# Kernel optimization log

Hardware: AMD Instinct MI355X
Metric: run time of the kernel (lower is better)

## Reference

```python
import jax, jax.numpy as jnp
import numpy as np

NEG_SLOPE = 0.2


def setup_inputs() -> dict:
    key = jax.random.key(0)
    ks = jax.random.split(key, 10)
    V, E, Din, Dout, H = 50000, 800000, 128, 128, 4
    h = jax.random.normal(ks[0], (V, Din), dtype=jnp.float32)
    edge_index = jax.random.randint(ks[1], (2, E), 0, V, dtype=jnp.int32)
    edge_weight = jax.random.uniform(ks[2], (E,), dtype=jnp.float32)
    s = 1.0 / np.sqrt(Din)
    Wq = jax.random.normal(ks[3], (Din, Dout), dtype=jnp.float32) * s
    Wk = jax.random.normal(ks[4], (Din, Dout), dtype=jnp.float32) * s
    Wv = jax.random.normal(ks[5], (Din, Dout), dtype=jnp.float32) * s
    Wo = jax.random.normal(ks[6], (Dout, Dout), dtype=jnp.float32) * (1.0 / np.sqrt(Dout))
    We = jax.random.normal(ks[7], (1, H), dtype=jnp.float32)
    bq = jnp.zeros((Dout,), jnp.float32)
    bk = jnp.zeros((Dout,), jnp.float32)
    bv = jnp.zeros((Dout,), jnp.float32)
    bo = jnp.zeros((Dout,), jnp.float32)
    be = jnp.zeros((H,), jnp.float32)
    return {"h": h, "edge_index": edge_index, "edge_weight": edge_weight,
            "Wq": Wq, "bq": bq, "Wk": Wk, "bk": bk, "Wv": Wv, "bv": bv,
            "Wo": Wo, "bo": bo, "We": We, "be": be}


def reference(h, edge_index, edge_weight, Wq, bq, Wk, bk, Wv, bv, Wo, bo, We, be):
    V = h.shape[0]
    H = be.shape[0]
    Dout = Wq.shape[1]
    F_h = Dout // H

    # Node projections -> [V, H, F_h]
    Q = (h @ Wq + bq).reshape(V, H, F_h)
    K = (h @ Wk + bk).reshape(V, H, F_h)
    Vv = (h @ Wv + bv).reshape(V, H, F_h)

    # Edge bias: Linear(1, H) on edge_weight, then LeakyReLU -> [E, H]
    edge_bias = jax.nn.leaky_relu(edge_weight[:, None] @ We + be, negative_slope=NEG_SLOPE)

    src, tgt = edge_index[0], edge_index[1]

    # Per-edge attention logits: dot(Q[src], K[tgt]) / sqrt(F_h) + bias -> [E, H]
    attn_raw = jnp.sum(Q[src] * K[tgt], axis=-1) / jnp.sqrt(jnp.float32(F_h)) + edge_bias
    attn_exp = jnp.exp(attn_raw)  # faithful: original uses unshifted exp

    # Scatter-softmax normalizer per target node -> [V, H]
    deg = jax.ops.segment_sum(attn_exp, tgt, num_segments=V) + 1e-16
    attn_norm = attn_exp / deg[tgt]  # [E, H]

    # Weighted messages and scatter-sum to targets
    msg = Vv[src] * attn_norm[:, :, None] * edge_weight[:, None, None]  # [E, H, F_h]
    out = jax.ops.segment_sum(msg, tgt, num_segments=V)  # [V, H, F_h]

    out = out.reshape(V, H * F_h)
    out = jax.nn.leaky_relu(out @ Wo + bo, negative_slope=NEG_SLOPE)
    return out
```

## Files before the change

### kernel.cpp

```cpp
#include <hip/hip_runtime.h>
#include <hip/hip_bf16.h>

#define NEG_SLOPE 0.2f

__global__ __launch_bounds__(256) void gemm_big(
    const float* __restrict__ A,
    const float* __restrict__ W0, const float* __restrict__ W1, const float* __restrict__ W2,
    const float* __restrict__ b0, const float* __restrict__ b1, const float* __restrict__ b2,
    float* __restrict__ D0, float* __restrict__ D1, float* __restrict__ D2,
    int V, int lrelu)
{
    __shared__ float As[16][136];
    __shared__ float Bs[16][192];

    const int m = blockIdx.y;
    const float* __restrict__ W  = (m == 0) ? W0 : ((m == 1) ? W1 : W2);
    const float* __restrict__ bb = (m == 0) ? b0 : ((m == 1) ? b1 : b2);
    float* __restrict__ D        = (m == 0) ? D0 : ((m == 1) ? D1 : D2);

    const int tid = threadIdx.x;
    const int tx = tid & 15;
    const int ty = tid >> 4;
    const int row0 = blockIdx.x * 128;

    const int ar = tid >> 1;
    const int ak = (tid & 1) * 8;
    const int bk = tid >> 4;
    const int bc = tid & 15;

    float acc[8][8];
#pragma unroll
    for (int i = 0; i < 8; ++i)
#pragma unroll
        for (int j = 0; j < 8; ++j) acc[i][j] = 0.f;

    for (int k0 = 0; k0 < 128; k0 += 16) {
        {
            const int gr = row0 + ar;
            float4 a0 = make_float4(0.f, 0.f, 0.f, 0.f);
            float4 a1 = make_float4(0.f, 0.f, 0.f, 0.f);
            if (gr < V) {
                a0 = *(const float4*)(A + (size_t)gr * 128 + k0 + ak);
                a1 = *(const float4*)(A + (size_t)gr * 128 + k0 + ak + 4);
            }
            As[ak + 0][ar] = a0.x; As[ak + 1][ar] = a0.y;
            As[ak + 2][ar] = a0.z; As[ak + 3][ar] = a0.w;
            As[ak + 4][ar] = a1.x; As[ak + 5][ar] = a1.y;
            As[ak + 6][ar] = a1.z; As[ak + 7][ar] = a1.w;
        }
        {
            const float4 w0 = *(const float4*)(W + (size_t)(k0 + bk) * 128 + bc * 8);
            const float4 w1 = *(const float4*)(W + (size_t)(k0 + bk) * 128 + bc * 8 + 4);
            *(float4*)&Bs[bk][bc * 12]     = w0;
            *(float4*)&Bs[bk][bc * 12 + 4] = w1;
        }
        __syncthreads();
#pragma unroll
        for (int kk = 0; kk < 16; ++kk) {
            float a[8], b[8];
            *(float4*)&a[0] = *(const float4*)&As[kk][ty * 8];
            *(float4*)&a[4] = *(const float4*)&As[kk][ty * 8 + 4];
            *(float4*)&b[0] = *(const float4*)&Bs[kk][tx * 12];
            *(float4*)&b[4] = *(const float4*)&Bs[kk][tx * 12 + 4];
#pragma unroll
            for (int i = 0; i < 8; ++i)
#pragma unroll
                for (int j = 0; j < 8; ++j) acc[i][j] = fmaf(a[i], b[j], acc[i][j]);
        }
        __syncthreads();
    }

#pragma unroll
    for (int i = 0; i < 8; ++i) {
        const int gr = row0 + ty * 8 + i;
        if (gr >= V) continue;
#pragma unroll
        for (int j = 0; j < 8; j += 4) {
            float4 o;
            float* op = &o.x;
#pragma unroll
            for (int jj = 0; jj < 4; ++jj) {
                float x = acc[i][j + jj] + bb[tx * 8 + j + jj];
                if (lrelu) x = (x > 0.f) ? x : NEG_SLOPE * x;
                op[jj] = x;
            }
            *(float4*)(D + (size_t)gr * 128 + tx * 8 + j) = o;
        }
    }
}

__global__ __launch_bounds__(256) void count_tgt(const int* __restrict__ tgt,
                                                 int* __restrict__ cnt, int E)
{
    const int e = blockIdx.x * blockDim.x + threadIdx.x;
    if (e < E) atomicAdd(cnt + tgt[e], 1);
}

__global__ __launch_bounds__(256) void scan1(const int* __restrict__ cnt,
                                             int* __restrict__ offs,
                                             int* __restrict__ bsums, int V)
{
    __shared__ int sh[256];
    const int t = threadIdx.x;
    const int base = blockIdx.x * 1024;
    int v[4];
    int s = 0;
#pragma unroll
    for (int i = 0; i < 4; ++i) {
        const int idx = base + t * 4 + i;
        v[i] = (idx < V) ? cnt[idx] : 0;
        s += v[i];
    }
    sh[t] = s;
    __syncthreads();
    for (int off = 1; off < 256; off <<= 1) {
        const int x = (t >= off) ? sh[t - off] : 0;
        __syncthreads();
        sh[t] += x;
        __syncthreads();
    }
    int run = (t > 0) ? sh[t - 1] : 0;
#pragma unroll
    for (int i = 0; i < 4; ++i) {
        const int idx = base + t * 4 + i;
        if (idx < V) offs[idx] = run;
        run += v[i];
    }
    if (t == 255) bsums[blockIdx.x] = sh[255];
}

__global__ void scan2(int* __restrict__ bsums, int nb)
{
    if (threadIdx.x == 0 && blockIdx.x == 0) {
        int run = 0;
        for (int i = 0; i < nb; ++i) { const int x = bsums[i]; bsums[i] = run; run += x; }
    }
}

__global__ __launch_bounds__(256) void scan3(int* __restrict__ offs,
                                             const int* __restrict__ bsums,
                                             int* __restrict__ fill, int V)
{
    const int v = blockIdx.x * blockDim.x + threadIdx.x;
    if (v >= V) return;
    const int o = offs[v] + bsums[v >> 10];
    offs[v] = o;
    fill[v] = o;
}

__global__ __launch_bounds__(256) void scatter_edges(
    const int* __restrict__ src, const int* __restrict__ tgt,
    const float* __restrict__ ew, int* __restrict__ fill,
    int2* __restrict__ se, int E)
{
    const int e = blockIdx.x * blockDim.x + threadIdx.x;
    if (e >= E) return;
    const int pos = atomicAdd(fill + tgt[e], 1);
    se[pos] = make_int2(src[e], __float_as_int(ew[e]));
}

__global__ __launch_bounds__(256) void fused_agg(
    const float* __restrict__ Q, const float* __restrict__ K,
    const float* __restrict__ Vv, const int2* __restrict__ se,
    const int* __restrict__ offs, const int* __restrict__ fill,
    const float* __restrict__ Wei, const float* __restrict__ bei,
    float* __restrict__ accum, int V)
{
    __shared__ float Ksh[4][4][36];
    const int wid = threadIdx.x >> 6;
    const int node = blockIdx.x * 4 + wid;
    if (node >= V) return;
    const int l   = threadIdx.x & 63;
    const int h   = l & 3;
    const int hd  = l >> 4;
    const float weH = Wei[h], beH = bei[h];
    const float2* __restrict__ Vv2 = (const float2*)Vv;

    {
        const float2 kk = *(const float2*)(K + (size_t)node * 128 + l * 2);
        const int f0 = l * 2;
        Ksh[wid][f0 >> 5][f0 & 31] = kk.x;
        Ksh[wid][(f0 + 1) >> 5][(f0 + 1) & 31] = kk.y;
    }

    const int start = offs[node];
    const int end   = fill[node];

    float degacc = 0.f;
    float ax = 0.f, ay = 0.f;

    for (int b0 = start; b0 < end; b0 += 16) {
        const int nj = min(16, end - b0);
        const int jj = l >> 2;
        int   s = 0;
        float w = 0.f, p = 0.f;
        if (jj < nj) {
            const int2 t = se[b0 + jj];
            s = t.x;
            w = __int_as_float(t.y);
            const float4* qp = (const float4*)(Q + (size_t)s * 128 + h * 32);
            float dot = 0.f;
#pragma unroll
            for (int i = 0; i < 8; ++i) {
                const float4 q = qp[i];
                const float4 k = *(const float4*)&Ksh[wid][h][i * 4];
                dot += q.x * k.x + q.y * k.y + q.z * k.z + q.w * k.w;
            }
            float bb = fmaf(w, weH, beH);
            bb = (bb > 0.f) ? bb : NEG_SLOPE * bb;
            p = __expf(fmaf(dot, 0.17677669529663687f, bb));
        }
        degacc += p;
        const float coef = p * w;

        if (nj == 16) {
#pragma unroll
            for (int j = 0; j < 16; ++j) {
                const float cj = __shfl(coef, j * 4 + hd);
                const int   sj = __shfl(s,    j * 4);
                const float2 v = Vv2[(size_t)sj * 64 + l];
                ax = fmaf(cj, v.x, ax);
                ay = fmaf(cj, v.y, ay);
            }
        } else {
            for (int j = 0; j < nj; ++j) {
                const float cj = __shfl(coef, j * 4 + hd);
                const int   sj = __shfl(s,    j * 4);
                const float2 v = Vv2[(size_t)sj * 64 + l];
                ax = fmaf(cj, v.x, ax);
                ay = fmaf(cj, v.y, ay);
            }
        }
    }

    float d = degacc;
    d += __shfl_xor(d, 4);
    d += __shfl_xor(d, 8);
    d += __shfl_xor(d, 16);
    d += __shfl_xor(d, 32);
    const float deg = __shfl(d, hd);
    const float inv = 1.0f / (deg + 1e-16f);

    *(float2*)(accum + (size_t)node * 128 + l * 2) =
        make_float2(ax * inv, ay * inv);
}

extern "C" void kernel_launch(void* const* d_in, const int* in_sizes, int n_in,
                              void* d_out, int out_size, void* d_ws, size_t ws_size,
                              hipStream_t stream)
{
    const float* h   = (const float*)d_in[0];
    const int*   ei  = (const int*)  d_in[1];
    const float* ew  = (const float*)d_in[2];
    const float* Wq  = (const float*)d_in[3];
    const float* bq  = (const float*)d_in[4];
    const float* Wk  = (const float*)d_in[5];
    const float* bk  = (const float*)d_in[6];
    const float* Wv  = (const float*)d_in[7];
    const float* bv  = (const float*)d_in[8];
    const float* Wo  = (const float*)d_in[9];
    const float* bo  = (const float*)d_in[10];
    const float* Wei = (const float*)d_in[11];
    const float* bei = (const float*)d_in[12];

    const int V = in_sizes[0] / 128;
    const int E = in_sizes[2];
    const int* src = ei;
    const int* tgt = ei + E;

    float* Q     = (float*)d_ws;
    float* Km    = Q  + (size_t)V * 128;
    float* Vm    = Km + (size_t)V * 128;
    float* accum = Vm + (size_t)V * 128;
    int2*  se    = (int2*)(accum + (size_t)V * 128);
    int*   cnt   = (int*)(se + E);
    int*   offs  = cnt  + V;
    int*   fill  = offs + V + 1;
    int*   bsums = fill + V;

    hipMemsetAsync(cnt, 0, (size_t)V * sizeof(int), stream);

    const int bigGrid = (V + 127) / 128;
    gemm_big<<<dim3(bigGrid, 3), 256, 0, stream>>>(
        h, Wq, Wk, Wv, bq, bk, bv, Q, Km, Vm, V, 0);

    count_tgt<<<(E + 255) / 256, 256, 0, stream>>>(tgt, cnt, E);
    const int nb = (V + 1023) / 1024;
    scan1<<<nb, 256, 0, stream>>>(cnt, offs, bsums, V);
    scan2<<<1, 64, 0, stream>>>(bsums, nb);
    scan3<<<(V + 255) / 256, 256, 0, stream>>>(offs, bsums, fill, V);
    scatter_edges<<<(E + 255) / 256, 256, 0, stream>>>(
        src, tgt, ew, fill, se, E);

    fused_agg<<<(V + 3) / 4, 256, 0, stream>>>(
        Q, Km, Vm, se, offs, fill, Wei, bei, accum, V);

    gemm_big<<<dim3(bigGrid, 1), 256, 0, stream>>>(
        accum, Wo, Wo, Wo, bo, bo, bo, (float*)d_out, (float*)d_out, (float*)d_out, V, 1);
}
```

Baseline: 319.0 us.

## Split aggregation per head so each wavefront handles one node-head pair

```diff
diff --git a/kernel.cpp b/kernel.cpp
--- a/kernel.cpp
+++ b/kernel.cpp
@@ -159,90 +159,85 @@
     se[pos] = make_int2(src[e], __float_as_int(ew[e]));
 }
 
-__global__ __launch_bounds__(256) void fused_agg(
+__global__ __launch_bounds__(256) void fused_agg_h(
     const float* __restrict__ Q, const float* __restrict__ K,
     const float* __restrict__ Vv, const int2* __restrict__ se,
     const int* __restrict__ offs, const int* __restrict__ fill,
     const float* __restrict__ Wei, const float* __restrict__ bei,
     float* __restrict__ accum, int V)
 {
-    __shared__ float Ksh[4][4][36];
-    const int wid = threadIdx.x >> 6;
-    const int node = blockIdx.x * 4 + wid;
+    const int head  = blockIdx.x & 3;
+    const int chunk = blockIdx.x >> 2;
+    const int wid   = threadIdx.x >> 6;
+    const int node  = chunk * 4 + wid;
     if (node >= V) return;
     const int l   = threadIdx.x & 63;
-    const int h   = l & 3;
-    const int hd  = l >> 4;
-    const float weH = Wei[h], beH = bei[h];
-    const float2* __restrict__ Vv2 = (const float2*)Vv;
-
-    {
-        const float2 kk = *(const float2*)(K + (size_t)node * 128 + l * 2);
-        const int f0 = l * 2;
-        Ksh[wid][f0 >> 5][f0 & 31] = kk.x;
-        Ksh[wid][(f0 + 1) >> 5][(f0 + 1) & 31] = kk.y;
-    }
-
-    const int start = offs[node];
-    const int end   = fill[node];
+    const int eg  = l >> 2;
+    const int qi  = l & 3;
+    const int grp = l >> 4;
+    const int d   = l & 15;
+
+    const float4* kp = (const float4*)(K + (size_t)node * 128 + head * 32);
+    const float4 k0 = kp[qi * 2];
+    const float4 k1 = kp[qi * 2 + 1];
+
+    const float weH = Wei[head], beH = bei[head];
+
+    int b0 = offs[node];
+    const int e0 = fill[node];
 
     float degacc = 0.f;
     float ax = 0.f, ay = 0.f;
 
-    for (int b0 = start; b0 < end; b0 += 16) {
-        const int nj = min(16, end - b0);
-        const int jj = l >> 2;
-        int   s = 0;
-        float w = 0.f, p = 0.f;
-        if (jj < nj) {
-            const int2 t = se[b0 + jj];
-            s = t.x;
-            w = __int_as_float(t.y);
-            const float4* qp = (const float4*)(Q + (size_t)s * 128 + h * 32);
-            float dot = 0.f;
-#pragma unroll
-            for (int i = 0; i < 8; ++i) {
-                const float4 q = qp[i];
-                const float4 k = *(const float4*)&Ksh[wid][h][i * 4];
-                dot += q.x * k.x + q.y * k.y + q.z * k.z + q.w * k.w;
+    for (; b0 < e0; b0 += 16) {
+        const int nj = min(16, e0 - b0);
+        int s_raw = 0; float w_raw = 0.f;
+        if (l < nj) {
+            const int2 t = se[b0 + l];
+            s_raw = t.x; w_raw = __int_as_float(t.y);
+        }
+        const int   s = __shfl(s_raw, eg);
+        const float w = __shfl(w_raw, eg);
+
+        float p = 0.f;
+        {
+            const float4* qp = (const float4*)(Q + (size_t)s * 128 + head * 32);
+            const float4 q0 = qp[qi * 2];
+            const float4 q1 = qp[qi * 2 + 1];
+            float dot = q0.x * k0.x + q0.y * k0.y + q0.z * k0.z + q0.w * k0.w
+                      + q1.x * k1.x + q1.y * k1.y + q1.z * k1.z + q1.w * k1.w;
+            dot += __shfl_xor(dot, 1);
+            dot += __shfl_xor(dot, 2);
+            if (eg < nj) {
+                float bb = fmaf(w, weH, beH);
+                bb = (bb > 0.f) ? bb : NEG_SLOPE * bb;
+                p = __expf(fmaf(dot, 0.17677669529663687f, bb));
             }
-            float bb = fmaf(w, weH, beH);
-            bb = (bb > 0.f) ? bb : NEG_SLOPE * bb;
-            p = __expf(fmaf(dot, 0.17677669529663687f, bb));
         }
         degacc += p;
         const float coef = p * w;
 
-        if (nj == 16) {
-#pragma unroll
-            for (int j = 0; j < 16; ++j) {
-                const float cj = __shfl(coef, j * 4 + hd);
-                const int   sj = __shfl(s,    j * 4);
-                const float2 v = Vv2[(size_t)sj * 64 + l];
-                ax = fmaf(cj, v.x, ax);
-                ay = fmaf(cj, v.y, ay);
-            }
-        } else {
-            for (int j = 0; j < nj; ++j) {
-                const float cj = __shfl(coef, j * 4 + hd);
-                const int   sj = __shfl(s,    j * 4);
-                const float2 v = Vv2[(size_t)sj * 64 + l];
-                ax = fmaf(cj, v.x, ax);
-                ay = fmaf(cj, v.y, ay);
-            }
-        }
-    }
-
-    float d = degacc;
-    d += __shfl_xor(d, 4);
-    d += __shfl_xor(d, 8);
-    d += __shfl_xor(d, 16);
-    d += __shfl_xor(d, 32);
-    const float deg = __shfl(d, hd);
-    const float inv = 1.0f / (deg + 1e-16f);
-
-    *(float2*)(accum + (size_t)node * 128 + l * 2) =
-        make_float2(ax * inv, ay * inv);
+        for (int j = 0; j < nj; j += 4) {
+            const int   e  = j + grp;
+            const float cj = __shfl(coef, e * 4);
+            const int   sj = __shfl(s,    e * 4);
+            const float2 v = *(const float2*)(Vv + (size_t)sj * 128 + head * 32 + d * 2);
+            ax = fmaf(cj, v.x, ax);
+            ay = fmaf(cj, v.y, ay);
+        }
+    }
+
+    ax += __shfl_xor(ax, 16); ax += __shfl_xor(ax, 32);
+    ay += __shfl_xor(ay, 16); ay += __shfl_xor(ay, 32);
+    float dg = degacc;
+    dg += __shfl_xor(dg, 1);  dg += __shfl_xor(dg, 2);
+    dg += __shfl_xor(dg, 4);  dg += __shfl_xor(dg, 8);
+    dg += __shfl_xor(dg, 16); dg += __shfl_xor(dg, 32);
+    const float inv = 1.0f / (dg * 0.25f + 1e-16f);
+
+    if (grp == 0)
+        *(float2*)(accum + (size_t)node * 128 + head * 32 + d * 2) =
+            make_float2(ax * inv, ay * inv);
 }
 
 extern "C" void kernel_launch(void* const* d_in, const int* in_sizes, int n_in,
@@ -292,7 +287,8 @@
     scatter_edges<<<(E + 255) / 256, 256, 0, stream>>>(
         src, tgt, ew, fill, se, E);
 
-    fused_agg<<<(V + 3) / 4, 256, 0, stream>>>(
+    const int chunks = (V + 3) / 4;
+    fused_agg_h<<<chunks * 4, 256, 0, stream>>>(
         Q, Km, Vm, se, offs, fill, Wei, bei, accum, V);
 
     gemm_big<<<dim3(bigGrid, 1), 256, 0, stream>>>(
```

After: 323.1 us. Within noise of the previous version (+1.3%).

## Replace FP32 SIMT GEMMs with split-bf16 MFMA GEMMs

Applied to the files above, without the earlier changes.

```diff
diff --git a/kernel.cpp b/kernel.cpp
--- a/kernel.cpp
+++ b/kernel.cpp
@@ -3,88 +3,122 @@
 
 #define NEG_SLOPE 0.2f
 
-__global__ __launch_bounds__(256) void gemm_big(
+typedef __attribute__((ext_vector_type(8))) short bf16x8;
+typedef __attribute__((ext_vector_type(4))) float f32x4;
+
+__device__ __forceinline__ void splitf(float x, unsigned short& h, unsigned short& l)
+{
+    const unsigned int u  = __float_as_uint(x);
+    const unsigned int uh = (u + 0x7fffu + ((u >> 16) & 1u)) >> 16;
+    const float        fh = __uint_as_float(uh << 16);
+    const float        r  = x - fh;
+    const unsigned int ur = __float_as_uint(r);
+    const unsigned int ul = (ur + 0x7fffu + ((ur >> 16) & 1u)) >> 16;
+    h = (unsigned short)uh;
+    l = (unsigned short)ul;
+}
+
+__global__ __launch_bounds__(256) void wsplit(const float* __restrict__ W,
+                                              unsigned short* __restrict__ Wth,
+                                              unsigned short* __restrict__ Wtl)
+{
+    const int t = blockIdx.x * 256 + threadIdx.x;
+    const int k = t >> 7, n = t & 127;
+    unsigned short h, l;
+    splitf(W[k * 128 + n], h, l);
+    Wth[n * 128 + k] = h;
+    Wtl[n * 128 + k] = l;
+}
+
+__global__ __launch_bounds__(256) void gemm_mfma(
     const float* __restrict__ A,
-    const float* __restrict__ W0, const float* __restrict__ W1, const float* __restrict__ W2,
+    const unsigned short* __restrict__ Bh0, const unsigned short* __restrict__ Bl0,
+    const unsigned short* __restrict__ Bh1, const unsigned short* __restrict__ Bl1,
+    const unsigned short* __restrict__ Bh2, const unsigned short* __restrict__ Bl2,
     const float* __restrict__ b0, const float* __restrict__ b1, const float* __restrict__ b2,
     float* __restrict__ D0, float* __restrict__ D1, float* __restrict__ D2,
     int V, int lrelu)
 {
-    __shared__ float As[16][136];
-    __shared__ float Bs[16][192];
+    __shared__ unsigned short Ash[64][40], Asl[64][40];
+    __shared__ unsigned short Bsh[128][40], Bsl[128][40];
 
     const int m = blockIdx.y;
-    const float* __restrict__ W  = (m == 0) ? W0 : ((m == 1) ? W1 : W2);
-    const float* __restrict__ bb = (m == 0) ? b0 : ((m == 1) ? b1 : b2);
-    float* __restrict__ D        = (m == 0) ? D0 : ((m == 1) ? D1 : D2);
-
-    const int tid = threadIdx.x;
-    const int tx = tid & 15;
-    const int ty = tid >> 4;
-    const int row0 = blockIdx.x * 128;
-
-    const int ar = tid >> 1;
-    const int ak = (tid & 1) * 8;
-    const int bk = tid >> 4;
-    const int bc = tid & 15;
-
-    float acc[8][8];
-#pragma unroll
-    for (int i = 0; i < 8; ++i)
-#pragma unroll
-        for (int j = 0; j < 8; ++j) acc[i][j] = 0.f;
-
-    for (int k0 = 0; k0 < 128; k0 += 16) {
+    const unsigned short* __restrict__ Wth = (m == 0) ? Bh0 : ((m == 1) ? Bh1 : Bh2);
+    const unsigned short* __restrict__ Wtl = (m == 0) ? Bl0 : ((m == 1) ? Bl1 : Bl2);
+    const float* __restrict__ bias         = (m == 0) ? b0  : ((m == 1) ? b1  : b2);
+    float* __restrict__ D                  = (m == 0) ? D0  : ((m == 1) ? D1  : D2);
+
+    const int tid  = threadIdx.x;
+    const int w    = tid >> 6;
+    const int l    = tid & 63;
+    const int row0 = blockIdx.x * 64;
+
+    const int srow = tid >> 2;
+    const int skc  = tid & 3;
+
+    f32x4 acc[8];
+#pragma unroll
+    for (int t = 0; t < 8; ++t) acc[t] = (f32x4){0.f, 0.f, 0.f, 0.f};
+
+    for (int k0 = 0; k0 < 128; k0 += 32) {
         {
-            const int gr = row0 + ar;
-            float4 a0 = make_float4(0.f, 0.f, 0.f, 0.f);
-            float4 a1 = make_float4(0.f, 0.f, 0.f, 0.f);
+            const int gr = row0 + srow;
+            float x[8] = {0.f, 0.f, 0.f, 0.f, 0.f, 0.f, 0.f, 0.f};
             if (gr < V) {
-                a0 = *(const float4*)(A + (size_t)gr * 128 + k0 + ak);
-                a1 = *(const float4*)(A + (size_t)gr * 128 + k0 + ak + 4);
-            }
-            As[ak + 0][ar] = a0.x; As[ak + 1][ar] = a0.y;
-            As[ak + 2][ar] = a0.z; As[ak + 3][ar] = a0.w;
-            As[ak + 4][ar] = a1.x; As[ak + 5][ar] = a1.y;
-            As[ak + 6][ar] = a1.z; As[ak + 7][ar] = a1.w;
-        }
-        {
-            const float4 w0 = *(const float4*)(W + (size_t)(k0 + bk) * 128 + bc * 8);
-            const float4 w1 = *(const float4*)(W + (size_t)(k0 + bk) * 128 + bc * 8 + 4);
-            *(float4*)&Bs[bk][bc * 12]     = w0;
-            *(float4*)&Bs[bk][bc * 12 + 4] = w1;
+                const float4 a0 = *(const float4*)(A + (size_t)gr * 128 + k0 + skc * 8);
+                const float4 a1 = *(const float4*)(A + (size_t)gr * 128 + k0 + skc * 8 + 4);
+                x[0] = a0.x; x[1] = a0.y; x[2] = a0.z; x[3] = a0.w;
+                x[4] = a1.x; x[5] = a1.y; x[6] = a1.z; x[7] = a1.w;
+            }
+            bf16x8 vh, vl;
+#pragma unroll
+            for (int i = 0; i < 8; ++i) {
+                unsigned short hh, ll;
+                splitf(x[i], hh, ll);
+                vh[i] = (short)hh; vl[i] = (short)ll;
+            }
+            *(bf16x8*)&Ash[srow][skc * 8] = vh;
+            *(bf16x8*)&Asl[srow][skc * 8] = vl;
+        }
+#pragma unroll
+        for (int r = 0; r < 2; ++r) {
+            const int idx = tid + r * 256;
+            const int n = idx >> 2, bkc = idx & 3;
+            *(bf16x8*)&Bsh[n][bkc * 8] = *(const bf16x8*)(Wth + n * 128 + k0 + bkc * 8);
+            *(bf16x8*)&Bsl[n][bkc * 8] = *(const bf16x8*)(Wtl + n * 128 + k0 + bkc * 8);
         }
         __syncthreads();
-#pragma unroll
-        for (int kk = 0; kk < 16; ++kk) {
-            float a[8], b[8];
-            *(float4*)&a[0] = *(const float4*)&As[kk][ty * 8];
-            *(float4*)&a[4] = *(const float4*)&As[kk][ty * 8 + 4];
-            *(float4*)&b[0] = *(const float4*)&Bs[kk][tx * 12];
-            *(float4*)&b[4] = *(const float4*)&Bs[kk][tx * 12 + 4];
-#pragma unroll
-            for (int i = 0; i < 8; ++i)
-#pragma unroll
-                for (int j = 0; j < 8; ++j) acc[i][j] = fmaf(a[i], b[j], acc[i][j]);
+
+        const int ar  = w * 16 + (l & 15);
+        const int kc8 = (l >> 4) * 8;
+        const bf16x8 ah = *(const bf16x8*)&Ash[ar][kc8];
+        const bf16x8 al = *(const bf16x8*)&Asl[ar][kc8];
+#pragma unroll
+        for (int t = 0; t < 8; ++t) {
+            const int col = t * 16 + (l & 15);
+            const bf16x8 bh = *(const bf16x8*)&Bsh[col][kc8];
+            const bf16x8 bl = *(const bf16x8*)&Bsl[col][kc8];
+            acc[t] = __builtin_amdgcn_mfma_f32_16x16x32_bf16(ah, bh, acc[t], 0, 0, 0);
+            acc[t] = __builtin_amdgcn_mfma_f32_16x16x32_bf16(ah, bl, acc[t], 0, 0, 0);
+            acc[t] = __builtin_amdgcn_mfma_f32_16x16x32_bf16(al, bh, acc[t], 0, 0, 0);
         }
         __syncthreads();
     }
 
-#pragma unroll
-    for (int i = 0; i < 8; ++i) {
-        const int gr = row0 + ty * 8 + i;
-        if (gr >= V) continue;
-#pragma unroll
-        for (int j = 0; j < 8; j += 4) {
-            float4 o;
-            float* op = &o.x;
-#pragma unroll
-            for (int jj = 0; jj < 4; ++jj) {
-                float x = acc[i][j + jj] + bb[tx * 8 + j + jj];
-                if (lrelu) x = (x > 0.f) ? x : NEG_SLOPE * x;
-                op[jj] = x;
-            }
-            *(float4*)(D + (size_t)gr * 128 + tx * 8 + j) = o;
+    const int colb = l & 15;
+    const int rsub = (l >> 4) * 4;
+#pragma unroll
+    for (int t = 0; t < 8; ++t) {
+        const int col = t * 16 + colb;
+        const float bv = bias[col];
+#pragma unroll
+        for (int r = 0; r < 4; ++r) {
+            const int grow = row0 + w * 16 + rsub + r;
+            if (grow < V) {
+                float xx = acc[t][r] + bv;
+                if (lrelu) xx = (xx > 0.f) ? xx : NEG_SLOPE * xx;
+                D[(size_t)grow * 128 + col] = xx;
+            }
         }
     }
 }
@@ -272,7 +306,16 @@
     float* Km    = Q  + (size_t)V * 128;
     float* Vm    = Km + (size_t)V * 128;
     float* accum = Vm + (size_t)V * 128;
-    int2*  se    = (int2*)(accum + (size_t)V * 128);
+    unsigned short* Wsp = (unsigned short*)(accum + (size_t)V * 128);
+    unsigned short* WthQ = Wsp;
+    unsigned short* WtlQ = Wsp + 16384;
+    unsigned short* WthK = Wsp + 2 * 16384;
+    unsigned short* WtlK = Wsp + 3 * 16384;
+    unsigned short* WthV = Wsp + 4 * 16384;
+    unsigned short* WtlV = Wsp + 5 * 16384;
+    unsigned short* WthO = Wsp + 6 * 16384;
+    unsigned short* WtlO = Wsp + 7 * 16384;
+    int2*  se    = (int2*)(Wsp + 8 * 16384);
     int*   cnt   = (int*)(se + E);
     int*   offs  = cnt  + V;
     int*   fill  = offs + V + 1;
@@ -280,9 +323,15 @@
 
     hipMemsetAsync(cnt, 0, (size_t)V * sizeof(int), stream);
 
-    const int bigGrid = (V + 127) / 128;
-    gemm_big<<<dim3(bigGrid, 3), 256, 0, stream>>>(
-        h, Wq, Wk, Wv, bq, bk, bv, Q, Km, Vm, V, 0);
+    wsplit<<<64, 256, 0, stream>>>(Wq, WthQ, WtlQ);
+    wsplit<<<64, 256, 0, stream>>>(Wk, WthK, WtlK);
+    wsplit<<<64, 256, 0, stream>>>(Wv, WthV, WtlV);
+    wsplit<<<64, 256, 0, stream>>>(Wo, WthO, WtlO);
+
+    const int mfGrid = (V + 63) / 64;
+    gemm_mfma<<<dim3(mfGrid, 3), 256, 0, stream>>>(
+        h, WthQ, WtlQ, WthK, WtlK, WthV, WtlV,
+        bq, bk, bv, Q, Km, Vm, V, 0);
 
     count_tgt<<<(E + 255) / 256, 256, 0, stream>>>(tgt, cnt, E);
     const int nb = (V + 1023) / 1024;
@@ -295,6 +344,7 @@
     fused_agg<<<(V + 3) / 4, 256, 0, stream>>>(
         Q, Km, Vm, se, offs, fill, Wei, bei, accum, V);
 
-    gemm_big<<<dim3(bigGrid, 1), 256, 0, stream>>>(
-        accum, Wo, Wo, Wo, bo, bo, bo, (float*)d_out, (float*)d_out, (float*)d_out, V, 1);
-}
+    gemm_mfma<<<dim3(mfGrid, 1), 256, 0, stream>>>(
+        accum, WthO, WtlO, WthO, WtlO, WthO, WtlO,
+        bo, bo, bo, (float*)d_out, (float*)d_out, (float*)d_out, V, 1);
+}
```

Result: faster. 294.7 us (-7.6%).
